# Performance work log

Hardware: AMD Instinct MI355X
Metric: run time of the kernel (lower is better)

Reference implementation:

```python
import jax, jax.numpy as jnp
import numpy as np

TWO_PI = 2.0 * np.pi

def _round_ste(y):
    # forward: round(y); backward: identity (straight-through), matching _RoundSTE
    return y + jax.lax.stop_gradient(jnp.round(y) - y)

def _anti_wrap(x):
    return jnp.abs(x - _round_ste(x / TWO_PI) * TWO_PI)

def setup_inputs() -> dict:
    key = jax.random.key(0)
    k1, k2 = jax.random.split(key)
    B, F, T = 32, 513, 1600  # F = n_fft//2 + 1 with n_fft=1024
    phase_r = jax.random.normal(k1, (B, F, T), dtype=jnp.float32)
    phase_g = jax.random.normal(k2, (B, F, T), dtype=jnp.float32)
    return {"phase_r": phase_r, "phase_g": phase_g}

def reference(phase_r, phase_g):
    # d[b,f,t] = phase_r - phase_g
    d = phase_r - phase_g
    ip_loss = jnp.mean(_anti_wrap(d))

    # GD_matrix has -1 on diag, +1 on superdiag; matmul(phase^T, M)[b,t,f]
    # = phase[b,f-1,t] - phase[b,f,t] (with implicit zero at f=-1).
    # GD_r - GD_g is the same banded diff applied to d along freq axis.
    d_shift_f = jnp.pad(d, ((0, 0), (1, 0), (0, 0)))[:, :-1, :]  # d[b,f-1,t], 0 at f=0
    gd_loss = jnp.mean(_anti_wrap(d_shift_f - d))

    # PTD_matrix: same banded diff along time axis.
    d_shift_t = jnp.pad(d, ((0, 0), (0, 0), (1, 0)))[:, :, :-1]  # d[b,f,t-1], 0 at t=0
    ptd_loss = jnp.mean(_anti_wrap(d_shift_t - d))

    return (ip_loss, gd_loss, ptd_loss)
```

## Files before the change

kernel.cpp:

```cpp
#include <hip/hip_runtime.h>
#include <math.h>

constexpr int Bc = 32, Fc = 513, Tc = 1600;
constexpr int BLK = 128;
constexpr int VEC = 4;
constexpr int TT  = BLK * VEC;
constexpr int NTT = (Tc + TT - 1) / TT;
constexpr int FCH = 27;
constexpr int NFC = Fc / FCH;
constexpr int NBLK = Bc * NFC * NTT;
constexpr long long NTOT = (long long)Bc * Fc * Tc;

typedef float f32x2 __attribute__((ext_vector_type(2)));

__device__ __forceinline__ f32x2 pk_fma(f32x2 a, f32x2 b, f32x2 c) {
    f32x2 d;
    asm("v_pk_fma_f32 %0, %1, %2, %3" : "=v"(d) : "v"(a), "v"(b), "v"(c));
    return d;
}
__device__ __forceinline__ f32x2 pk_add(f32x2 a, f32x2 b) {
    f32x2 d;
    asm("v_pk_add_f32 %0, %1, %2" : "=v"(d) : "v"(a), "v"(b));
    return d;
}

#define INV2PI 0.15915494309189535f
#define MAGICF 12582912.0f
#define N2PI  -6.283185307179586f

__device__ __forceinline__ void aw_acc(f32x2 x, float& sA, float& sB,
                                       f32x2 cinv, f32x2 cmag, f32x2 cnmag,
                                       f32x2 cn2pi) {
    f32x2 y = pk_fma(x, cinv, cmag);
    f32x2 r = pk_add(y, cnmag);
    f32x2 w = pk_fma(r, cn2pi, x);
    sA += fabsf(w.x);
    sB += fabsf(w.y);
}

__device__ __forceinline__ void block_reduce3(float& a, float& b, float& c) {
    #pragma unroll
    for (int off = 32; off > 0; off >>= 1) {
        a += __shfl_down(a, off);
        b += __shfl_down(b, off);
        c += __shfl_down(c, off);
    }
    __shared__ float sm[3][BLK / 64];
    const int lane = threadIdx.x & 63, wid = threadIdx.x >> 6;
    if (lane == 0) { sm[0][wid] = a; sm[1][wid] = b; sm[2][wid] = c; }
    __syncthreads();
    if (threadIdx.x == 0) {
        a = sm[0][0]; b = sm[1][0]; c = sm[2][0];
        #pragma unroll
        for (int w = 1; w < BLK / 64; ++w) {
            a += sm[0][w]; b += sm[1][w]; c += sm[2][w];
        }
    }
}

__global__ __launch_bounds__(BLK) void phase_main(
        const float* __restrict__ pr, const float* __restrict__ pg,
        float* __restrict__ partials,
        float* __restrict__ out,
        int use_atomic)
{
    const int tile = blockIdx.x;
    const int fc   = blockIdx.y;
    const int b    = blockIdx.z;
    const int t0   = tile * TT + (int)threadIdx.x * VEC;
    const int f0   = fc * FCH;
    const int f1   = f0 + FCH;
    const int lane = (int)threadIdx.x & 63;
    const bool edge = (lane == 0) && (t0 > 0);

    const f32x2 cneg1 = {-1.0f, -1.0f};
    const f32x2 cinv  = {INV2PI, INV2PI};
    const f32x2 cmag  = {MAGICF, MAGICF};
    const f32x2 cnmag = {-MAGICF, -MAGICF};
    const f32x2 cn2pi = {N2PI, N2PI};

    float ipA = 0.f, ipB = 0.f, gdA = 0.f, gdB = 0.f, ptA = 0.f, ptB = 0.f;

    if (t0 < Tc) {
        const size_t baseb = (size_t)b * Fc * Tc + (size_t)t0;
        const float* ap = pr + baseb + (size_t)f0 * Tc;
        const float* gp = pg + baseb + (size_t)f0 * Tc;

        f32x2 pd01, pd23;
        if (f0 == 0) {
            pd01 = (f32x2){0.f, 0.f}; pd23 = (f32x2){0.f, 0.f};
        } else {
            float4 a = *(const float4*)(ap - Tc);
            float4 g = *(const float4*)(gp - Tc);
            pd01 = (f32x2){a.x - g.x, a.y - g.y};
            pd23 = (f32x2){a.z - g.z, a.w - g.w};
        }

        float4 aC = *(const float4*)ap;
        float4 gC = *(const float4*)gp;
        float4 aN = *(const float4*)(ap + Tc);
        float4 gN = *(const float4*)(gp + Tc);
        float amC = 0.f, gmC = 0.f, amN = 0.f, gmN = 0.f;
        if (edge) {
            amC = ap[-1];      gmC = gp[-1];
            amN = ap[Tc - 1];  gmN = gp[Tc - 1];
        }

        #pragma unroll 3
        for (int f = f0; f < f1; ++f) {
            const bool ok = (f + 2 < f1);
            const float* ap2 = ok ? (ap + 2 * (size_t)Tc) : ap;
            const float* gp2 = ok ? (gp + 2 * (size_t)Tc) : gp;
            float4 aP = *(const float4*)ap2;
            float4 gP = *(const float4*)gp2;
            float amP = 0.f, gmP = 0.f;
            if (edge) { amP = ap2[-1]; gmP = gp2[-1]; }

            f32x2 a01 = {aC.x, aC.y}, a23 = {aC.z, aC.w};
            f32x2 g01 = {gC.x, gC.y}, g23 = {gC.z, gC.w};
            f32x2 d01 = pk_fma(g01, cneg1, a01);
            f32x2 d23 = pk_fma(g23, cneg1, a23);

            float dwm = __shfl_up(d23.y, 1);
            float dm1 = (lane == 0) ? (amC - gmC) : dwm;

            f32x2 sh01 = {dm1, d01.x};
            f32x2 sh23 = {d01.y, d23.x};
            f32x2 pdd01 = pk_fma(d01, cneg1, pd01);
            f32x2 pdd23 = pk_fma(d23, cneg1, pd23);
            f32x2 tdd01 = pk_fma(d01, cneg1, sh01);
            f32x2 tdd23 = pk_fma(d23, cneg1, sh23);

            aw_acc(d01,  ipA, ipB, cinv, cmag, cnmag, cn2pi);
            aw_acc(d23,  ipA, ipB, cinv, cmag, cnmag, cn2pi);
            aw_acc(pdd01, gdA, gdB, cinv, cmag, cnmag, cn2pi);
            aw_acc(pdd23, gdA, gdB, cinv, cmag, cnmag, cn2pi);
            aw_acc(tdd01, ptA, ptB, cinv, cmag, cnmag, cn2pi);
            aw_acc(tdd23, ptA, ptB, cinv, cmag, cnmag, cn2pi);

            pd01 = d01; pd23 = d23;
            aC = aN; gC = gN; amC = amN; gmC = gmN;
            aN = aP; gN = gP; amN = amP; gmN = gmP;
            ap += Tc; gp += Tc;
        }
    }

    float s_ip = ipA + ipB, s_gd = gdA + gdB, s_ptd = ptA + ptB;
    block_reduce3(s_ip, s_gd, s_ptd);

    if (threadIdx.x == 0) {
        if (use_atomic) {
            const float invN = (float)(1.0 / (double)NTOT);
            atomicAdd(out + 0, s_ip * invN);
            atomicAdd(out + 1, s_gd * invN);
            atomicAdd(out + 2, s_ptd * invN);
        } else {
            const int bid = (blockIdx.z * gridDim.y + blockIdx.y) * gridDim.x
                          + blockIdx.x;
            partials[0 * NBLK + bid] = s_ip;
            partials[1 * NBLK + bid] = s_gd;
            partials[2 * NBLK + bid] = s_ptd;
        }
    }
}

__global__ __launch_bounds__(256) void phase_reduce(
        const float* __restrict__ partials, float* __restrict__ out)
{
    const int c = blockIdx.x;
    const int tid = threadIdx.x;
    float s = 0.f;
    for (int i = tid; i < NBLK; i += 256) s += partials[(size_t)c * NBLK + i];
    #pragma unroll
    for (int off = 32; off > 0; off >>= 1) s += __shfl_down(s, off);
    __shared__ float sm[4];
    const int lane = tid & 63, wid = tid >> 6;
    if (lane == 0) sm[wid] = s;
    __syncthreads();
    if (tid == 0) {
        float t = sm[0] + sm[1] + sm[2] + sm[3];
        out[c] = t * (float)(1.0 / (double)NTOT);
    }
}

__global__ void zero3(float* out) {
    if (threadIdx.x < 3) out[threadIdx.x] = 0.f;
}

extern "C" void kernel_launch(void* const* d_in, const int* in_sizes, int n_in,
                              void* d_out, int out_size, void* d_ws, size_t ws_size,
                              hipStream_t stream) {
    const float* pr = (const float*)d_in[0];
    const float* pg = (const float*)d_in[1];
    float* out = (float*)d_out;
    dim3 grid(NTT, NFC, Bc);

    if (ws_size >= (size_t)NBLK * 3 * sizeof(float)) {
        float* partials = (float*)d_ws;
        phase_main<<<grid, BLK, 0, stream>>>(pr, pg, partials, nullptr, 0);
        phase_reduce<<<3, 256, 0, stream>>>(partials, out);
    } else {
        zero3<<<1, 64, 0, stream>>>(out);
        phase_main<<<grid, BLK, 0, stream>>>(pr, pg, nullptr, out, 1);
    }
}
```

Measured before the change: 49.25 us.

## Assign full time rows per wavefront over short frequency strips

The grid is remapped so each 64-lane wavefront owns one batch and an 8-row frequency strip. It covers all 1600 time samples in registers, using cross-lane shuffles to carry the time-shift neighbour between chunks. This removes the idle threads in the old partial last time tile and the scalar halo loads at tile edges. In exchange, the previous frequency row is reloaded once per 8 rows instead of once per 27, and register pressure rises from holding seven float4 chunks per row. The grid also shrinks to fewer, larger blocks.

```diff
diff --git a/kernel.cpp b/kernel.cpp
--- a/kernel.cpp
+++ b/kernel.cpp
@@ -2,13 +2,12 @@
 #include <math.h>
 
 constexpr int Bc = 32, Fc = 513, Tc = 1600;
-constexpr int BLK = 128;
-constexpr int VEC = 4;
-constexpr int TT  = BLK * VEC;
-constexpr int NTT = (Tc + TT - 1) / TT;
-constexpr int FCH = 27;
-constexpr int NFC = Fc / FCH;
-constexpr int NBLK = Bc * NFC * NTT;
+constexpr int FCH = 8;
+constexpr int SPB = 65;
+constexpr int NSTRIP = Bc * SPB;
+constexpr int WPB = 4;
+constexpr int BLK = 64 * WPB;
+constexpr int NBLK = NSTRIP / WPB;
 constexpr long long NTOT = (long long)Bc * Fc * Tc;
 
 typedef float f32x2 __attribute__((ext_vector_type(2)));
@@ -21,6 +20,11 @@
 __device__ __forceinline__ f32x2 pk_add(f32x2 a, f32x2 b) {
     f32x2 d;
     asm("v_pk_add_f32 %0, %1, %2" : "=v"(d) : "v"(a), "v"(b));
+    return d;
+}
+__device__ __forceinline__ f32x2 pk_mul(f32x2 a, f32x2 b) {
+    f32x2 d;
+    asm("v_pk_mul_f32 %0, %1, %2" : "=v"(d) : "v"(a), "v"(b));
     return d;
 }
 
@@ -38,128 +42,133 @@
     sB += fabsf(w.y);
 }
 
-__device__ __forceinline__ void block_reduce3(float& a, float& b, float& c) {
-    #pragma unroll
-    for (int off = 32; off > 0; off >>= 1) {
-        a += __shfl_down(a, off);
-        b += __shfl_down(b, off);
-        c += __shfl_down(c, off);
-    }
-    __shared__ float sm[3][BLK / 64];
-    const int lane = threadIdx.x & 63, wid = threadIdx.x >> 6;
-    if (lane == 0) { sm[0][wid] = a; sm[1][wid] = b; sm[2][wid] = c; }
-    __syncthreads();
-    if (threadIdx.x == 0) {
-        a = sm[0][0]; b = sm[1][0]; c = sm[2][0];
-        #pragma unroll
-        for (int w = 1; w < BLK / 64; ++w) {
-            a += sm[0][w]; b += sm[1][w]; c += sm[2][w];
-        }
-    }
-}
-
 __global__ __launch_bounds__(BLK) void phase_main(
         const float* __restrict__ pr, const float* __restrict__ pg,
         float* __restrict__ partials,
         float* __restrict__ out,
         int use_atomic)
 {
-    const int tile = blockIdx.x;
-    const int fc   = blockIdx.y;
-    const int b    = blockIdx.z;
-    const int t0   = tile * TT + (int)threadIdx.x * VEC;
-    const int f0   = fc * FCH;
-    const int f1   = f0 + FCH;
     const int lane = (int)threadIdx.x & 63;
-    const bool edge = (lane == 0) && (t0 > 0);
+    const int wv   = (int)blockIdx.x * WPB + ((int)threadIdx.x >> 6);
+    const int b    = wv / SPB;
+    const int k    = wv - b * SPB;
+    const int f0   = k * FCH;
+    const int len  = (k == SPB - 1) ? 1 : FCH;
+
+    const size_t rowbase = ((size_t)b * Fc + (size_t)f0) * Tc;
+    const float* ap = pr + rowbase;
+    const float* gp = pg + rowbase;
 
     const f32x2 cneg1 = {-1.0f, -1.0f};
     const f32x2 cinv  = {INV2PI, INV2PI};
     const f32x2 cmag  = {MAGICF, MAGICF};
     const f32x2 cnmag = {-MAGICF, -MAGICF};
     const f32x2 cn2pi = {N2PI, N2PI};
+    const float mtail = (lane < 16) ? 1.0f : 0.0f;
+    const f32x2 m2    = {mtail, mtail};
 
     float ipA = 0.f, ipB = 0.f, gdA = 0.f, gdB = 0.f, ptA = 0.f, ptB = 0.f;
 
-    if (t0 < Tc) {
-        const size_t baseb = (size_t)b * Fc * Tc + (size_t)t0;
-        const float* ap = pr + baseb + (size_t)f0 * Tc;
-        const float* gp = pg + baseb + (size_t)f0 * Tc;
-
-        f32x2 pd01, pd23;
-        if (f0 == 0) {
-            pd01 = (f32x2){0.f, 0.f}; pd23 = (f32x2){0.f, 0.f};
-        } else {
-            float4 a = *(const float4*)(ap - Tc);
-            float4 g = *(const float4*)(gp - Tc);
-            pd01 = (f32x2){a.x - g.x, a.y - g.y};
-            pd23 = (f32x2){a.z - g.z, a.w - g.w};
-        }
-
-        float4 aC = *(const float4*)ap;
-        float4 gC = *(const float4*)gp;
-        float4 aN = *(const float4*)(ap + Tc);
-        float4 gN = *(const float4*)(gp + Tc);
-        float amC = 0.f, gmC = 0.f, amN = 0.f, gmN = 0.f;
-        if (edge) {
-            amC = ap[-1];      gmC = gp[-1];
-            amN = ap[Tc - 1];  gmN = gp[Tc - 1];
-        }
-
-        #pragma unroll 3
-        for (int f = f0; f < f1; ++f) {
-            const bool ok = (f + 2 < f1);
-            const float* ap2 = ok ? (ap + 2 * (size_t)Tc) : ap;
-            const float* gp2 = ok ? (gp + 2 * (size_t)Tc) : gp;
-            float4 aP = *(const float4*)ap2;
-            float4 gP = *(const float4*)gp2;
-            float amP = 0.f, gmP = 0.f;
-            if (edge) { amP = ap2[-1]; gmP = gp2[-1]; }
-
-            f32x2 a01 = {aC.x, aC.y}, a23 = {aC.z, aC.w};
-            f32x2 g01 = {gC.x, gC.y}, g23 = {gC.z, gC.w};
-            f32x2 d01 = pk_fma(g01, cneg1, a01);
-            f32x2 d23 = pk_fma(g23, cneg1, a23);
-
-            float dwm = __shfl_up(d23.y, 1);
-            float dm1 = (lane == 0) ? (amC - gmC) : dwm;
-
-            f32x2 sh01 = {dm1, d01.x};
-            f32x2 sh23 = {d01.y, d23.x};
-            f32x2 pdd01 = pk_fma(d01, cneg1, pd01);
-            f32x2 pdd23 = pk_fma(d23, cneg1, pd23);
+    float4 A[7], G[7], Dc[7], Dp[7];
+
+    auto load_row = [&](const float* p, float4* R) {
+        #pragma unroll
+        for (int c = 0; c < 6; ++c)
+            R[c] = *(const float4*)(p + c * 256 + lane * 4);
+        if (lane < 16) R[6] = *(const float4*)(p + 1536 + lane * 4);
+        else           R[6] = make_float4(0.f, 0.f, 0.f, 0.f);
+    };
+    auto diff7 = [&](float4* D, const float4* X, const float4* Y) {
+        #pragma unroll
+        for (int c = 0; c < 7; ++c) {
+            f32x2 x01 = {X[c].x, X[c].y}, x23 = {X[c].z, X[c].w};
+            f32x2 y01 = {Y[c].x, Y[c].y}, y23 = {Y[c].z, Y[c].w};
+            f32x2 d01 = pk_fma(y01, cneg1, x01);
+            f32x2 d23 = pk_fma(y23, cneg1, x23);
+            D[c] = make_float4(d01.x, d01.y, d23.x, d23.y);
+        }
+    };
+    auto acc_row = [&](const float4* D, const float4* P) {
+        #pragma unroll
+        for (int c = 0; c < 7; ++c) {
+            f32x2 d01 = {D[c].x, D[c].y}, d23 = {D[c].z, D[c].w};
+            f32x2 p01 = {P[c].x, P[c].y}, p23 = {P[c].z, P[c].w};
+            float up    = __shfl_up(D[c].w, 1);
+            float carry = (c == 0) ? 0.f : __shfl(D[c - 1].w, 63);
+            float dm1   = (lane == 0) ? carry : up;
+            f32x2 sh01 = {dm1, D[c].x};
+            f32x2 sh23 = {D[c].y, D[c].z};
+            f32x2 pdd01 = pk_fma(d01, cneg1, p01);
+            f32x2 pdd23 = pk_fma(d23, cneg1, p23);
             f32x2 tdd01 = pk_fma(d01, cneg1, sh01);
             f32x2 tdd23 = pk_fma(d23, cneg1, sh23);
-
+            if (c == 6) {
+                tdd01 = pk_mul(tdd01, m2);
+                tdd23 = pk_mul(tdd23, m2);
+            }
             aw_acc(d01,  ipA, ipB, cinv, cmag, cnmag, cn2pi);
             aw_acc(d23,  ipA, ipB, cinv, cmag, cnmag, cn2pi);
             aw_acc(pdd01, gdA, gdB, cinv, cmag, cnmag, cn2pi);
             aw_acc(pdd23, gdA, gdB, cinv, cmag, cnmag, cn2pi);
             aw_acc(tdd01, ptA, ptB, cinv, cmag, cnmag, cn2pi);
             aw_acc(tdd23, ptA, ptB, cinv, cmag, cnmag, cn2pi);
-
-            pd01 = d01; pd23 = d23;
-            aC = aN; gC = gN; amC = amN; gmC = gmN;
-            aN = aP; gN = gP; amN = amP; gmN = gmP;
-            ap += Tc; gp += Tc;
+        }
+    };
+
+    load_row(ap, A);
+    load_row(gp, G);
+    if (f0 > 0) {
+        float4 Pa[7], Pg[7];
+        load_row(ap - Tc, Pa);
+        load_row(gp - Tc, Pg);
+        diff7(Dp, Pa, Pg);
+    } else {
+        #pragma unroll
+        for (int c = 0; c < 7; ++c) Dp[c] = make_float4(0.f, 0.f, 0.f, 0.f);
+    }
+    diff7(Dc, A, G);
+
+    if (len == 1) {
+        acc_row(Dc, Dp);
+    } else {
+        for (int i = 0; i < FCH; i += 2) {
+            const size_t o1 = (size_t)min(i + 1, FCH - 1) * Tc;
+            load_row(ap + o1, A);
+            load_row(gp + o1, G);
+            acc_row(Dc, Dp);
+            diff7(Dp, A, G);
+            const size_t o2 = (size_t)min(i + 2, FCH - 1) * Tc;
+            load_row(ap + o2, A);
+            load_row(gp + o2, G);
+            acc_row(Dp, Dc);
+            diff7(Dc, A, G);
         }
     }
 
     float s_ip = ipA + ipB, s_gd = gdA + gdB, s_ptd = ptA + ptB;
-    block_reduce3(s_ip, s_gd, s_ptd);
-
+    #pragma unroll
+    for (int off = 32; off > 0; off >>= 1) {
+        s_ip  += __shfl_down(s_ip, off);
+        s_gd  += __shfl_down(s_gd, off);
+        s_ptd += __shfl_down(s_ptd, off);
+    }
+    __shared__ float sm[3][WPB];
+    const int wid = (int)threadIdx.x >> 6;
+    if (lane == 0) { sm[0][wid] = s_ip; sm[1][wid] = s_gd; sm[2][wid] = s_ptd; }
+    __syncthreads();
     if (threadIdx.x == 0) {
+        float a = 0.f, bb = 0.f, c = 0.f;
+        #pragma unroll
+        for (int w = 0; w < WPB; ++w) { a += sm[0][w]; bb += sm[1][w]; c += sm[2][w]; }
         if (use_atomic) {
             const float invN = (float)(1.0 / (double)NTOT);
-            atomicAdd(out + 0, s_ip * invN);
-            atomicAdd(out + 1, s_gd * invN);
-            atomicAdd(out + 2, s_ptd * invN);
+            atomicAdd(out + 0, a * invN);
+            atomicAdd(out + 1, bb * invN);
+            atomicAdd(out + 2, c * invN);
         } else {
-            const int bid = (blockIdx.z * gridDim.y + blockIdx.y) * gridDim.x
-                          + blockIdx.x;
-            partials[0 * NBLK + bid] = s_ip;
-            partials[1 * NBLK + bid] = s_gd;
-            partials[2 * NBLK + bid] = s_ptd;
+            partials[0 * NBLK + blockIdx.x] = a;
+            partials[1 * NBLK + blockIdx.x] = bb;
+            partials[2 * NBLK + blockIdx.x] = c;
         }
     }
 }
@@ -193,14 +202,13 @@
     const float* pr = (const float*)d_in[0];
     const float* pg = (const float*)d_in[1];
     float* out = (float*)d_out;
-    dim3 grid(NTT, NFC, Bc);
 
     if (ws_size >= (size_t)NBLK * 3 * sizeof(float)) {
         float* partials = (float*)d_ws;
-        phase_main<<<grid, BLK, 0, stream>>>(pr, pg, partials, nullptr, 0);
+        phase_main<<<NBLK, BLK, 0, stream>>>(pr, pg, partials, nullptr, 0);
         phase_reduce<<<3, 256, 0, stream>>>(partials, out);
     } else {
         zero3<<<1, 64, 0, stream>>>(out);
-        phase_main<<<grid, BLK, 0, stream>>>(pr, pg, nullptr, out, 1);
-    }
-}
+        phase_main<<<NBLK, BLK, 0, stream>>>(pr, pg, nullptr, out, 1);
+    }
+}
```

Result: faster. 48.01 us, median of 2 (-2.5%).
